# Optimization experiments

Measured on AMD Instinct MI355X. Metric: run time of the kernel, lower is better.

Reference implementation:

```python
import jax, jax.numpy as jnp
import numpy as np

N_HEADS = 16
MAX_SEQ_LEN = 2048


def _rotary_tables(d_k, max_seq_len):
    # Rotary.__init__: dim//4 frequencies followed by dim//4 zeros -> dim//2 entries
    freqs = (1.0 / 10000.0) ** jnp.linspace(0.0, 1.0, d_k // 4, dtype=jnp.float32)
    freqs = jnp.concatenate([freqs, jnp.zeros(d_k // 4, dtype=jnp.float32)])
    theta = jnp.arange(max_seq_len, dtype=jnp.float32)[:, None] * freqs[None, :]  # [S, d_k//2]
    return jnp.cos(theta), jnp.sin(theta)


def _apply_rotary_bug_faithful(u, cos, sin):
    # u: [B, H, T, Dk]. Original Rotary indexes cos/sin by u.size(-3) == n_heads,
    # so the rotation angle depends on the HEAD index and broadcasts over time.
    H = u.shape[1]
    c = cos[None, :H, None, :]  # [1, H, 1, Dk//2]
    s = sin[None, :H, None, :]
    u1, u2 = jnp.split(u.astype(jnp.float32), 2, axis=-1)
    y1 = u1 * c + u2 * s
    y2 = -u1 * s + u2 * c
    return jnp.concatenate([y1, y2], axis=-1).astype(u.dtype)


def setup_inputs() -> dict:
    key = jax.random.key(0)
    k1, k2, k3 = jax.random.split(key, 3)
    d_model = 2048
    B, T = 2, 2048
    x = jax.random.normal(k1, (B, T, d_model), dtype=jnp.float32)
    w_qkv = jax.random.normal(k2, (3 * d_model, d_model), dtype=jnp.float32) * (1.0 / np.sqrt(d_model))
    w_o = jax.random.normal(k3, (d_model, d_model), dtype=jnp.float32) * (1.0 / np.sqrt(d_model))
    return {"x": x, "w_qkv": w_qkv, "w_o": w_o}


def reference(x, w_qkv, w_o):
    B, T, D = x.shape
    H = N_HEADS
    dk = D // H
    cos, sin = _rotary_tables(dk, MAX_SEQ_LEN)

    # Fused QKV projection (Linear, no bias): [B,T,3D]
    qkv = jnp.einsum('btd,ed->bte', x, w_qkv)
    qkv = qkv.reshape(B, T, 3, H, dk).transpose(2, 0, 3, 1, 4)  # [3,B,H,T,dk]
    Q, K, V = qkv[0], qkv[1], qkv[2]

    Q = _apply_rotary_bug_faithful(Q, cos, sin)
    K = _apply_rotary_bug_faithful(K, cos, sin)

    # Causal scaled dot-product attention (eval mode -> dropout_p = 0)
    scale = 1.0 / np.sqrt(dk)
    scores = jnp.einsum('bhqd,bhkd->bhqk', Q, K) * scale
    causal = jnp.tril(jnp.ones((T, T), dtype=bool))
    scores = jnp.where(causal[None, None], scores, jnp.finfo(scores.dtype).min)
    attn = jax.nn.softmax(scores, axis=-1)
    out = jnp.einsum('bhqk,bhkd->bhqd', attn, V)  # [B,H,T,dk]
    out = out.transpose(0, 2, 1, 3).reshape(B, T, D)
    return jnp.einsum('btd,ed->bte', out, w_o)
```

## Files before the change

kernel.cpp:

```cpp
#include <hip/hip_runtime.h>

typedef unsigned short u16;
typedef short bf16x8 __attribute__((ext_vector_type(8)));
typedef float f32x4 __attribute__((ext_vector_type(4)));
typedef unsigned short u16x4 __attribute__((ext_vector_type(4)));

#define QK_SCALE 0.08838834764831845f

__device__ __forceinline__ u16 f2bf(float f) {
  unsigned u = __float_as_uint(f);
  u += 0x7fffu + ((u >> 16) & 1u);
  return (u16)(u >> 16);
}
__device__ __forceinline__ float bf2f(u16 h) { return __uint_as_float(((unsigned)h) << 16); }

__device__ __forceinline__ void gld_lds16(const u16* g, u16* l) {
  __builtin_amdgcn_global_load_lds(
      (const __attribute__((address_space(1))) void*)g,
      (__attribute__((address_space(3))) void*)l, 16, 0, 0);
}

__global__ void cvt_bf16_kernel(const float* __restrict__ in, u16* __restrict__ out, int n4) {
  int i = blockIdx.x * 256 + threadIdx.x;
  if (i >= n4) return;
  const float4 v = reinterpret_cast<const float4*>(in)[i];
  u16x4 o;
  o[0] = f2bf(v.x); o[1] = f2bf(v.y); o[2] = f2bf(v.z); o[3] = f2bf(v.w);
  reinterpret_cast<u16x4*>(out)[i] = o;
}

template<int MODE>
__global__ __launch_bounds__(512, 2) void gemm8p_kernel(
    const u16* __restrict__ A, const u16* __restrict__ Bw, int Kdim, int n_out,
    u16* __restrict__ q_out, u16* __restrict__ k_out, u16* __restrict__ v_out,
    float* __restrict__ f_out)
{
  __shared__ __align__(16) u16 As[2][256 * 64];
  __shared__ __align__(16) u16 Bs[2][256 * 64];
  const int t = threadIdx.x, lane = t & 63, w = t >> 6;
  const int wr = w >> 2, wc = w & 3;
  const int l15 = lane & 15, lhi = lane >> 4;
  const int m0 = blockIdx.x * 256, n0 = blockIdx.y * 256;
  const int NT = Kdim >> 6;

  const int srow = w * 8 + (lane >> 3);
  const int gchunk = (lane & 7) ^ (srow & 7);
  const size_t gcol = (size_t)gchunk * 8;

  auto stageA2 = [&](int buf, int kt2, int half) {
    const size_t kb = (size_t)kt2 * 64 + gcol;
#pragma unroll
    for (int i = 0; i < 2; ++i) {
      const int ro = half * 128 + i * 64;
      gld_lds16(A + (size_t)(m0 + srow + ro) * Kdim + kb, &As[buf][(w * 8 + ro) * 64]);
    }
  };
  auto stageB4 = [&](int buf, int kt2) {
    const size_t kb = (size_t)kt2 * 64 + gcol;
#pragma unroll
    for (int ro = 0; ro < 256; ro += 64)
      gld_lds16(Bw + (size_t)(n0 + srow + ro) * Kdim + kb, &Bs[buf][(w * 8 + ro) * 64]);
  };

  const int arow0 = (wr * 128 + l15) * 64;
  const int brow0 = (wc * 64 + l15) * 64;
  const int koff0 = ((0 + lhi) ^ (l15 & 7)) * 8;
  const int koff1 = ((4 + lhi) ^ (l15 & 7)) * 8;

  f32x4 acc[8][4];
#pragma unroll
  for (int m = 0; m < 8; ++m)
#pragma unroll
    for (int n = 0; n < 4; ++n)
#pragma unroll
      for (int i = 0; i < 4; ++i) acc[m][n][i] = 0.0f;

  stageA2(0, 0, 0); stageA2(0, 0, 1);
  stageB4(0, 0);
  if (NT > 1) { stageA2(1, 1, 0); stageA2(1, 1, 1); }
  asm volatile("s_waitcnt vmcnt(4)" ::: "memory");
  __builtin_amdgcn_s_barrier();

  for (int kt = 0; kt < NT; ++kt) {
    const int cur = kt & 1;
    const u16* __restrict__ Ac = &As[cur][0];
    const u16* __restrict__ Bc = &Bs[cur][0];
    bf16x8 aK1[4], a2K1[4], b0[4], b1[4];
    {
      bf16x8 aK0[4];
#pragma unroll
      for (int m = 0; m < 4; ++m) {
        aK0[m] = *reinterpret_cast<const bf16x8*>(Ac + arow0 + m * 1024 + koff0);
        aK1[m] = *reinterpret_cast<const bf16x8*>(Ac + arow0 + m * 1024 + koff1);
      }
#pragma unroll
      for (int n = 0; n < 4; ++n)
        b0[n] = *reinterpret_cast<const bf16x8*>(Bc + brow0 + n * 1024 + koff0);
      if (kt + 1 < NT) stageB4(cur ^ 1, kt + 1);
      __builtin_amdgcn_s_barrier();
      asm volatile("s_waitcnt lgkmcnt(0)" ::: "memory");
      __builtin_amdgcn_s_setprio(1);
#pragma unroll
      for (int m = 0; m < 4; ++m)
#pragma unroll
        for (int n = 0; n < 4; ++n)
          acc[m][n] = __builtin_amdgcn_mfma_f32_16x16x32_bf16(aK0[m], b0[n], acc[m][n], 0, 0, 0);
      __builtin_amdgcn_s_setprio(0);
      __builtin_amdgcn_s_barrier();
    }
    {
      bf16x8 a2K0[4];
#pragma unroll
      for (int m = 0; m < 4; ++m) {
        a2K0[m] = *reinterpret_cast<const bf16x8*>(Ac + arow0 + (m + 4) * 1024 + koff0);
        a2K1[m] = *reinterpret_cast<const bf16x8*>(Ac + arow0 + (m + 4) * 1024 + koff1);
      }
#pragma unroll
      for (int n = 0; n < 4; ++n)
        b1[n] = *reinterpret_cast<const bf16x8*>(Bc + brow0 + n * 1024 + koff1);
      __builtin_amdgcn_s_barrier();
      asm volatile("s_waitcnt lgkmcnt(0)" ::: "memory");
      __builtin_amdgcn_s_setprio(1);
#pragma unroll
      for (int m = 0; m < 4; ++m)
#pragma unroll
        for (int n = 0; n < 4; ++n)
          acc[m + 4][n] = __builtin_amdgcn_mfma_f32_16x16x32_bf16(a2K0[m], b0[n], acc[m + 4][n], 0, 0, 0);
      __builtin_amdgcn_s_setprio(0);
      __builtin_amdgcn_s_barrier();
    }
    if (kt + 2 < NT) stageA2(cur, kt + 2, 0);
    __builtin_amdgcn_s_barrier();
    __builtin_amdgcn_s_setprio(1);
#pragma unroll
    for (int m = 0; m < 4; ++m)
#pragma unroll
      for (int n = 0; n < 4; ++n)
        acc[m][n] = __builtin_amdgcn_mfma_f32_16x16x32_bf16(aK1[m], b1[n], acc[m][n], 0, 0, 0);
    __builtin_amdgcn_s_setprio(0);
    __builtin_amdgcn_s_barrier();
    if (kt + 2 < NT) stageA2(cur, kt + 2, 1);
    __builtin_amdgcn_s_barrier();
    __builtin_amdgcn_s_setprio(1);
#pragma unroll
    for (int m = 0; m < 4; ++m)
#pragma unroll
      for (int n = 0; n < 4; ++n)
        acc[m + 4][n] = __builtin_amdgcn_mfma_f32_16x16x32_bf16(a2K1[m], b1[n], acc[m + 4][n], 0, 0, 0);
    __builtin_amdgcn_s_setprio(0);
    if (kt < NT - 2) { asm volatile("s_waitcnt vmcnt(4)" ::: "memory"); }
    else             { asm volatile("s_waitcnt vmcnt(0)" ::: "memory"); }
    __builtin_amdgcn_s_barrier();
  }

  const int rb = wr * 128 + lhi * 4;
  const int cb = wc * 64 + l15;
  if (MODE == 0) {
#pragma unroll
    for (int n = 0; n < 4; ++n) {
      const int e = n0 + cb + n * 16;
      const int which = e >> 11;
      const int h = (e >> 7) & 15;
      const int d = e & 127;
      u16* dst = (which == 0) ? q_out : (which == 1) ? k_out : v_out;
#pragma unroll
      for (int m = 0; m < 8; ++m)
#pragma unroll
        for (int r = 0; r < 4; ++r) {
          const int bt = m0 + rb + m * 16 + r;
          const int bb = bt >> 11, tt = bt & 2047;
          dst[((size_t)(bb * 16 + h) * 2048 + tt) * 128 + d] = f2bf(acc[m][n][r]);
        }
    }
  } else {
#pragma unroll
    for (int m = 0; m < 8; ++m)
#pragma unroll
      for (int r = 0; r < 4; ++r) {
        const int row = m0 + rb + m * 16 + r;
#pragma unroll
        for (int n = 0; n < 4; ++n)
          f_out[(size_t)row * n_out + n0 + cb + n * 16] = acc[m][n][r];
      }
  }
}

__global__ __launch_bounds__(256) void gemm_bt_kernel(
    const u16* __restrict__ A, const u16* __restrict__ Bw, int Kdim, int n_out,
    float* __restrict__ f_out)
{
  __shared__ __align__(16) u16 Asl[128 * 32];
  __shared__ __align__(16) u16 Bsl[128 * 32];
  const int t = threadIdx.x;
  const int lane = t & 63;
  const int w = t >> 6;
  const int wr = w >> 1, wc = w & 1;
  const int m0 = blockIdx.x * 128, n0 = blockIdx.y * 128;

  f32x4 acc[4][4];
#pragma unroll
  for (int m = 0; m < 4; ++m)
#pragma unroll
    for (int n = 0; n < 4; ++n)
#pragma unroll
      for (int i = 0; i < 4; ++i) acc[m][n][i] = 0.0f;

  const int ob0 = w * 1024 + lane * 16;
  const int row0 = ob0 >> 6;
  const int cole0 = (ob0 & 63) >> 1;
  const u16* gA0 = A + (size_t)(m0 + row0) * Kdim + cole0;
  const u16* gA1 = gA0 + (size_t)64 * Kdim;
  const u16* gB0 = Bw + (size_t)(n0 + row0) * Kdim + cole0;
  const u16* gB1 = gB0 + (size_t)64 * Kdim;
  u16* lA = Asl + w * 512;
  u16* lB = Bsl + w * 512;

  const int l15 = lane & 15;
  const int kb = (lane >> 4) * 8;

  for (int k0 = 0; k0 < Kdim; k0 += 32) {
    __syncthreads();
    gld_lds16(gA0, lA);
    gld_lds16(gA1, lA + 2048);
    gld_lds16(gB0, lB);
    gld_lds16(gB1, lB + 2048);
    gA0 += 32; gA1 += 32; gB0 += 32; gB1 += 32;
    __syncthreads();
    bf16x8 a[4], b[4];
#pragma unroll
    for (int m = 0; m < 4; ++m)
      a[m] = *reinterpret_cast<const bf16x8*>(Asl + (wr * 64 + m * 16 + l15) * 32 + kb);
#pragma unroll
    for (int n = 0; n < 4; ++n)
      b[n] = *reinterpret_cast<const bf16x8*>(Bsl + (wc * 64 + n * 16 + l15) * 32 + kb);
#pragma unroll
    for (int m = 0; m < 4; ++m)
#pragma unroll
      for (int n = 0; n < 4; ++n)
        acc[m][n] = __builtin_amdgcn_mfma_f32_16x16x32_bf16(a[m], b[n], acc[m][n], 0, 0, 0);
  }

  const int rb = wr * 64 + ((lane >> 4) << 2);
  const int cbs = wc * 64 + l15;
#pragma unroll
  for (int m = 0; m < 4; ++m)
#pragma unroll
    for (int r = 0; r < 4; ++r) {
      const int row = m0 + rb + m * 16 + r;
#pragma unroll
      for (int n = 0; n < 4; ++n)
        f_out[(size_t)row * n_out + n0 + cbs + n * 16] = acc[m][n][r];
    }
}

__global__ void rotary_kernel(u16* __restrict__ Qb, u16* __restrict__ Kb) {
  const int idx = blockIdx.x * 256 + threadIdx.x;
  const int j4 = idx & 15;
  const int row = idx >> 4;
  const int h = (row >> 11) & 15;
  const size_t base = (size_t)row * 128 + j4 * 4;
  float c[4], s[4];
#pragma unroll
  for (int i = 0; i < 4; ++i) {
    const int j = j4 * 4 + i;
    const float fr = (j < 32) ? __expf(-0.2971077539f * (float)j) : 0.0f;
    const float th = (float)h * fr;
    c[i] = cosf(th); s[i] = sinf(th);
  }
  {
    u16x4 u1 = *reinterpret_cast<u16x4*>(Qb + base);
    u16x4 u2 = *reinterpret_cast<u16x4*>(Qb + base + 64);
    u16x4 y1, y2;
#pragma unroll
    for (int i = 0; i < 4; ++i) {
      const float a = bf2f(u1[i]), b = bf2f(u2[i]);
      y1[i] = f2bf((a * c[i] + b * s[i]) * QK_SCALE);
      y2[i] = f2bf((b * c[i] - a * s[i]) * QK_SCALE);
    }
    *reinterpret_cast<u16x4*>(Qb + base) = y1;
    *reinterpret_cast<u16x4*>(Qb + base + 64) = y2;
  }
  {
    u16x4 u1 = *reinterpret_cast<u16x4*>(Kb + base);
    u16x4 u2 = *reinterpret_cast<u16x4*>(Kb + base + 64);
    u16x4 y1, y2;
#pragma unroll
    for (int i = 0; i < 4; ++i) {
      const float a = bf2f(u1[i]), b = bf2f(u2[i]);
      y1[i] = f2bf(a * c[i] + b * s[i]);
      y2[i] = f2bf(b * c[i] - a * s[i]);
    }
    *reinterpret_cast<u16x4*>(Kb + base) = y1;
    *reinterpret_cast<u16x4*>(Kb + base + 64) = y2;
  }
}

__global__ void transpose_v_kernel(const u16* __restrict__ V, u16* __restrict__ Vt) {
  __shared__ u16 tile[64][65];
  const int d0 = blockIdx.x * 64;
  const int t0 = blockIdx.y * 64;
  const int bh = blockIdx.z;
  const u16* src = V + (size_t)bh * (2048 * 128);
  u16* dst = Vt + (size_t)bh * (128 * 2048);
  const int tid = threadIdx.x;
  const int c4 = (tid & 15) * 4;
  const int r0 = tid >> 4;
#pragma unroll
  for (int p = 0; p < 4; ++p) {
    const int row = r0 + p * 16;
    const u16x4 v = *reinterpret_cast<const u16x4*>(src + (size_t)(t0 + row) * 128 + d0 + c4);
    tile[row][c4] = v[0]; tile[row][c4 + 1] = v[1];
    tile[row][c4 + 2] = v[2]; tile[row][c4 + 3] = v[3];
  }
  __syncthreads();
#pragma unroll
  for (int p = 0; p < 4; ++p) {
    const int dr = r0 + p * 16;
    u16x4 ov;
    ov[0] = tile[c4][dr]; ov[1] = tile[c4 + 1][dr];
    ov[2] = tile[c4 + 2][dr]; ov[3] = tile[c4 + 3][dr];
    *reinterpret_cast<u16x4*>(dst + (size_t)(d0 + dr) * 2048 + t0 + c4) = ov;
  }
}

__global__ __launch_bounds__(256) void attn_kernel(
    const u16* __restrict__ Q, const u16* __restrict__ K,
    const u16* __restrict__ Vt, u16* __restrict__ O)
{
  __shared__ __align__(16) u16 k_lds[2][64 * 128];
  __shared__ __align__(16) u16 v_lds[2][128 * 64];
  __shared__ __align__(16) u16 p_lds[4][1024];
  const int t = threadIdx.x, lane = t & 63, w = t >> 6;
  const int bh = blockIdx.y;
  const int bx = blockIdx.x;
  const int l15 = lane & 15, lhi = lane >> 4;
  const size_t qkb = (size_t)bh * (2048 * 128);
  const u16* Kg = K + qkb;
  const u16* Vg = Vt + (size_t)bh * (size_t)(128 * 2048);
  char* pw = (char*)(&p_lds[w][0]);
  const int bb = bh >> 4, h = bh & 15;
  const int kxor = (l15 & 7) << 4;

  auto stage = [&](int buf, int k0) {
#pragma unroll
    for (int ii = 0; ii < 4; ++ii) {
      const int i = w * 4 + ii;
      const int krow = i * 4 + lhi;
      gld_lds16(Kg + (size_t)(k0 + krow) * 128 + (size_t)((l15 ^ (krow & 7)) * 8),
                &k_lds[buf][i * 512]);
    }
#pragma unroll
    for (int ii = 0; ii < 4; ++ii) {
      const int i = w * 4 + ii;
      const int vrow = i * 8 + (lane >> 3);
      gld_lds16(Vg + (size_t)vrow * 2048 + k0 + (size_t)(((lane & 7) ^ (vrow & 7)) * 8),
                &v_lds[buf][i * 512]);
    }
  };

  for (int half = 0; half < 2; ++half) {
    const int qt = half ? (31 - bx) : bx;
    const int q0 = qt * 64 + w * 16;
    bf16x8 aq[4];
    {
      const u16* qp = Q + qkb + (size_t)(q0 + l15) * 128 + lhi * 8;
#pragma unroll
      for (int ks = 0; ks < 4; ++ks) aq[ks] = *reinterpret_cast<const bf16x8*>(qp + ks * 32);
    }
    f32x4 o[8];
#pragma unroll
    for (int dt = 0; dt < 8; ++dt)
#pragma unroll
      for (int i = 0; i < 4; ++i) o[dt][i] = 0.0f;
    float mrow[4] = {-1e30f, -1e30f, -1e30f, -1e30f};
    float lrow[4] = {0.f, 0.f, 0.f, 0.f};
    const int rbase = q0 + (lhi << 2);
    const int ktmax = qt;

    __syncthreads();
    stage(0, 0);
    int cur = 0;
    for (int kt = 0; kt <= ktmax; ++kt) {
      __syncthreads();
      if (kt < ktmax) stage(cur ^ 1, (kt + 1) * 64);

      const char* kbb = (const char*)(&k_lds[cur][0]);
      f32x4 s4[4];
#pragma unroll
      for (int nt = 0; nt < 4; ++nt)
#pragma unroll
        for (int i = 0; i < 4; ++i) s4[nt][i] = 0.0f;
#pragma unroll
      for (int nt = 0; nt < 4; ++nt) {
        const int krow = nt * 16 + l15;
#pragma unroll
        for (int ks = 0; ks < 4; ++ks) {
          const bf16x8 bk = *reinterpret_cast<const bf16x8*>(
              kbb + krow * 256 + ((ks * 64 + lhi * 16) ^ kxor));
          s4[nt] = __builtin_amdgcn_mfma_f32_16x16x32_bf16(aq[ks], bk, s4[nt], 0, 0, 0);
        }
      }
      if (kt == ktmax) {
#pragma unroll
        for (int nt = 0; nt < 4; ++nt) {
          const int col = kt * 64 + nt * 16 + l15;
#pragma unroll
          for (int r = 0; r < 4; ++r)
            if (col > rbase + r) s4[nt][r] = -1e30f;
        }
      }
      float alpha[4];
#pragma unroll
      for (int r = 0; r < 4; ++r) {
        float mx = fmaxf(fmaxf(s4[0][r], s4[1][r]), fmaxf(s4[2][r], s4[3][r]));
        mx = fmaxf(mx, __shfl_xor(mx, 1));
        mx = fmaxf(mx, __shfl_xor(mx, 2));
        mx = fmaxf(mx, __shfl_xor(mx, 4));
        mx = fmaxf(mx, __shfl_xor(mx, 8));
        const float mn = fmaxf(mrow[r], mx);
        alpha[r] = __expf(mrow[r] - mn);
        mrow[r] = mn;
      }
      float ps[4] = {0.f, 0.f, 0.f, 0.f};
#pragma unroll
      for (int nt = 0; nt < 4; ++nt)
#pragma unroll
        for (int r = 0; r < 4; ++r) {
          const float p = __expf(s4[nt][r] - mrow[r]);
          ps[r] += p;
          const int prow = (lhi << 2) + r;
          const int cbyte = (nt * 16 + l15) * 2;
          *(u16*)(pw + prow * 128 + (cbyte ^ ((prow & 7) << 4))) = f2bf(p);
        }
#pragma unroll
      for (int r = 0; r < 4; ++r) {
        float rs = ps[r];
        rs += __shfl_xor(rs, 1);
        rs += __shfl_xor(rs, 2);
        rs += __shfl_xor(rs, 4);
        rs += __shfl_xor(rs, 8);
        lrow[r] = lrow[r] * alpha[r] + rs;
#pragma unroll
        for (int dt = 0; dt < 8; ++dt) o[dt][r] *= alpha[r];
      }
      const char* vbb = (const char*)(&v_lds[cur][0]);
#pragma unroll
      for (int ks2 = 0; ks2 < 2; ++ks2) {
        const bf16x8 ap = *reinterpret_cast<const bf16x8*>(
            pw + l15 * 128 + ((ks2 * 64 + (lhi << 4)) ^ kxor));
#pragma unroll
        for (int dt = 0; dt < 8; ++dt) {
          const int vrow = dt * 16 + l15;
          const bf16x8 bv = *reinterpret_cast<const bf16x8*>(
              vbb + vrow * 128 + ((ks2 * 64 + lhi * 16) ^ kxor));
          o[dt] = __builtin_amdgcn_mfma_f32_16x16x32_bf16(ap, bv, o[dt], 0, 0, 0);
        }
      }
      cur ^= 1;
    }
#pragma unroll
    for (int r = 0; r < 4; ++r) {
      const float inv = 1.0f / lrow[r];
      const int row = rbase + r;
      u16* op = O + (size_t)(bb * 2048 + row) * 2048 + h * 128 + l15;
#pragma unroll
      for (int dt = 0; dt < 8; ++dt) op[dt * 16] = f2bf(o[dt][r] * inv);
    }
  }
}

extern "C" void kernel_launch(void* const* d_in, const int* in_sizes, int n_in,
                              void* d_out, int out_size, void* d_ws, size_t ws_size,
                              hipStream_t stream) {
  const float* x = (const float*)d_in[0];
  const float* wqkv = (const float*)d_in[1];
  const float* wo = (const float*)d_in[2];
  float* out = (float*)d_out;
  u16* ws = (u16*)d_ws;

  u16* xb = ws;
  u16* wqkvb = xb + 8388608;
  u16* wob = wqkvb + 12582912;
  u16* Qb = wob + 4194304;
  u16* Kb = Qb + 8388608;
  u16* Vb = Kb + 8388608;
  u16* Vtb = wqkvb;
  u16* attn = xb;

  cvt_bf16_kernel<<<8192, 256, 0, stream>>>(x, xb, 2097152);
  cvt_bf16_kernel<<<12288, 256, 0, stream>>>(wqkv, wqkvb, 3145728);
  cvt_bf16_kernel<<<4096, 256, 0, stream>>>(wo, wob, 1048576);

  gemm8p_kernel<0><<<dim3(16, 24), 512, 0, stream>>>(xb, wqkvb, 2048, 0, Qb, Kb, Vb, nullptr);

  rotary_kernel<<<4096, 256, 0, stream>>>(Qb, Kb);
  transpose_v_kernel<<<dim3(2, 32, 32), 256, 0, stream>>>(Vb, Vtb);

  attn_kernel<<<dim3(16, 32), 256, 0, stream>>>(Qb, Kb, Vtb, attn);

  gemm_bt_kernel<<<dim3(32, 16), 256, 0, stream>>>(attn, wob, 2048, 2048, out);
}
```

Measured before the change: 323.3 us.

## Fold rotary into QKV weights, write V transposed from GEMM, swizzle block order

New measurement: 346.7 us. 1.07x slower.

```diff
diff --git a/kernel.cpp b/kernel.cpp
--- a/kernel.cpp
+++ b/kernel.cpp
@@ -27,6 +27,33 @@
   u16x4 o;
   o[0] = f2bf(v.x); o[1] = f2bf(v.y); o[2] = f2bf(v.z); o[3] = f2bf(v.w);
   reinterpret_cast<u16x4*>(out)[i] = o;
+}
+
+__global__ void rotw_kernel(const float* __restrict__ w, u16* __restrict__ wb) {
+  const int i = blockIdx.x * 256 + threadIdx.x;
+  const int k4 = i & 511;
+  const int j = (i >> 9) & 63;
+  const int h = (i >> 15) & 15;
+  const int which = i >> 19;
+  const size_t e1 = (size_t)which * 2048 + h * 128 + j;
+  const size_t e2 = e1 + 64;
+  const float fr = (j < 32) ? __expf(-0.2971077539f * (float)j) : 0.0f;
+  float s, c;
+  __sincosf((float)h * fr, &s, &c);
+  const float scale = (which == 0) ? QK_SCALE : 1.0f;
+  const float4 a = reinterpret_cast<const float4*>(w + e1 * 2048)[k4];
+  const float4 b = reinterpret_cast<const float4*>(w + e2 * 2048)[k4];
+  u16x4 o1, o2;
+  o1[0] = f2bf((a.x * c + b.x * s) * scale);
+  o1[1] = f2bf((a.y * c + b.y * s) * scale);
+  o1[2] = f2bf((a.z * c + b.z * s) * scale);
+  o1[3] = f2bf((a.w * c + b.w * s) * scale);
+  o2[0] = f2bf((b.x * c - a.x * s) * scale);
+  o2[1] = f2bf((b.y * c - a.y * s) * scale);
+  o2[2] = f2bf((b.z * c - a.z * s) * scale);
+  o2[3] = f2bf((b.w * c - a.w * s) * scale);
+  reinterpret_cast<u16x4*>(wb + e1 * 2048)[k4] = o1;
+  reinterpret_cast<u16x4*>(wb + e2 * 2048)[k4] = o2;
 }
 
 template<int MODE>
@@ -40,7 +67,9 @@
   const int t = threadIdx.x, lane = t & 63, w = t >> 6;
   const int wr = w >> 2, wc = w & 3;
   const int l15 = lane & 15, lhi = lane >> 4;
-  const int m0 = blockIdx.x * 256, n0 = blockIdx.y * 256;
+  const int flat = blockIdx.y * 16 + blockIdx.x;
+  const int swz = (flat & 7) * 48 + (flat >> 3);
+  const int m0 = (swz & 15) << 8, n0 = (swz >> 4) << 8;
   const int NT = Kdim >> 6;
 
   const int srow = w * 8 + (lane >> 3);
@@ -162,14 +191,19 @@
       const int which = e >> 11;
       const int h = (e >> 7) & 15;
       const int d = e & 127;
-      u16* dst = (which == 0) ? q_out : (which == 1) ? k_out : v_out;
 #pragma unroll
       for (int m = 0; m < 8; ++m)
 #pragma unroll
         for (int r = 0; r < 4; ++r) {
           const int bt = m0 + rb + m * 16 + r;
           const int bb = bt >> 11, tt = bt & 2047;
-          dst[((size_t)(bb * 16 + h) * 2048 + tt) * 128 + d] = f2bf(acc[m][n][r]);
+          const float val = acc[m][n][r];
+          if (which == 2) {
+            v_out[((size_t)(bb * 16 + h) * 128 + d) * 2048 + tt] = f2bf(val);
+          } else {
+            u16* dst = (which == 0) ? q_out : k_out;
+            dst[((size_t)(bb * 16 + h) * 2048 + tt) * 128 + d] = f2bf(val);
+          }
         }
     }
   } else {
@@ -195,7 +229,9 @@
   const int lane = t & 63;
   const int w = t >> 6;
   const int wr = w >> 1, wc = w & 1;
-  const int m0 = blockIdx.x * 128, n0 = blockIdx.y * 128;
+  const int flat = blockIdx.y * 32 + blockIdx.x;
+  const int swz = (flat & 7) * 64 + (flat >> 3);
+  const int m0 = (swz & 31) << 7, n0 = (swz >> 5) << 7;
 
   f32x4 acc[4][4];
 #pragma unroll
@@ -253,76 +289,6 @@
     }
 }
 
-__global__ void rotary_kernel(u16* __restrict__ Qb, u16* __restrict__ Kb) {
-  const int idx = blockIdx.x * 256 + threadIdx.x;
-  const int j4 = idx & 15;
-  const int row = idx >> 4;
-  const int h = (row >> 11) & 15;
-  const size_t base = (size_t)row * 128 + j4 * 4;
-  float c[4], s[4];
-#pragma unroll
-  for (int i = 0; i < 4; ++i) {
-    const int j = j4 * 4 + i;
-    const float fr = (j < 32) ? __expf(-0.2971077539f * (float)j) : 0.0f;
-    const float th = (float)h * fr;
-    c[i] = cosf(th); s[i] = sinf(th);
-  }
-  {
-    u16x4 u1 = *reinterpret_cast<u16x4*>(Qb + base);
-    u16x4 u2 = *reinterpret_cast<u16x4*>(Qb + base + 64);
-    u16x4 y1, y2;
-#pragma unroll
-    for (int i = 0; i < 4; ++i) {
-      const float a = bf2f(u1[i]), b = bf2f(u2[i]);
-      y1[i] = f2bf((a * c[i] + b * s[i]) * QK_SCALE);
-      y2[i] = f2bf((b * c[i] - a * s[i]) * QK_SCALE);
-    }
-    *reinterpret_cast<u16x4*>(Qb + base) = y1;
-    *reinterpret_cast<u16x4*>(Qb + base + 64) = y2;
-  }
-  {
-    u16x4 u1 = *reinterpret_cast<u16x4*>(Kb + base);
-    u16x4 u2 = *reinterpret_cast<u16x4*>(Kb + base + 64);
-    u16x4 y1, y2;
-#pragma unroll
-    for (int i = 0; i < 4; ++i) {
-      const float a = bf2f(u1[i]), b = bf2f(u2[i]);
-      y1[i] = f2bf(a * c[i] + b * s[i]);
-      y2[i] = f2bf(b * c[i] - a * s[i]);
-    }
-    *reinterpret_cast<u16x4*>(Kb + base) = y1;
-    *reinterpret_cast<u16x4*>(Kb + base + 64) = y2;
-  }
-}
-
-__global__ void transpose_v_kernel(const u16* __restrict__ V, u16* __restrict__ Vt) {
-  __shared__ u16 tile[64][65];
-  const int d0 = blockIdx.x * 64;
-  const int t0 = blockIdx.y * 64;
-  const int bh = blockIdx.z;
-  const u16* src = V + (size_t)bh * (2048 * 128);
-  u16* dst = Vt + (size_t)bh * (128 * 2048);
-  const int tid = threadIdx.x;
-  const int c4 = (tid & 15) * 4;
-  const int r0 = tid >> 4;
-#pragma unroll
-  for (int p = 0; p < 4; ++p) {
-    const int row = r0 + p * 16;
-    const u16x4 v = *reinterpret_cast<const u16x4*>(src + (size_t)(t0 + row) * 128 + d0 + c4);
-    tile[row][c4] = v[0]; tile[row][c4 + 1] = v[1];
-    tile[row][c4 + 2] = v[2]; tile[row][c4 + 3] = v[3];
-  }
-  __syncthreads();
-#pragma unroll
-  for (int p = 0; p < 4; ++p) {
-    const int dr = r0 + p * 16;
-    u16x4 ov;
-    ov[0] = tile[c4][dr]; ov[1] = tile[c4 + 1][dr];
-    ov[2] = tile[c4 + 2][dr]; ov[3] = tile[c4 + 3][dr];
-    *reinterpret_cast<u16x4*>(dst + (size_t)(d0 + dr) * 2048 + t0 + c4) = ov;
-  }
-}
-
 __global__ __launch_bounds__(256) void attn_kernel(
     const u16* __restrict__ Q, const u16* __restrict__ K,
     const u16* __restrict__ Vt, u16* __restrict__ O)
@@ -331,8 +297,10 @@
   __shared__ __align__(16) u16 v_lds[2][128 * 64];
   __shared__ __align__(16) u16 p_lds[4][1024];
   const int t = threadIdx.x, lane = t & 63, w = t >> 6;
-  const int bh = blockIdx.y;
-  const int bx = blockIdx.x;
+  const int flat = blockIdx.y * 16 + blockIdx.x;
+  const int swz = (flat & 7) * 64 + (flat >> 3);
+  const int bx = swz & 15;
+  const int bh = swz >> 4;
   const int l15 = lane & 15, lhi = lane >> 4;
   const size_t qkb = (size_t)bh * (2048 * 128);
   const u16* Kg = K + qkb;
@@ -483,18 +451,16 @@
   u16* wob = wqkvb + 12582912;
   u16* Qb = wob + 4194304;
   u16* Kb = Qb + 8388608;
-  u16* Vb = Kb + 8388608;
-  u16* Vtb = wqkvb;
+  u16* Vtb = Kb + 8388608;
   u16* attn = xb;
 
   cvt_bf16_kernel<<<8192, 256, 0, stream>>>(x, xb, 2097152);
-  cvt_bf16_kernel<<<12288, 256, 0, stream>>>(wqkv, wqkvb, 3145728);
+  rotw_kernel<<<4096, 256, 0, stream>>>(wqkv, wqkvb);
+  cvt_bf16_kernel<<<4096, 256, 0, stream>>>(wqkv + (size_t)4096 * 2048,
+                                            wqkvb + (size_t)4096 * 2048, 1048576);
   cvt_bf16_kernel<<<4096, 256, 0, stream>>>(wo, wob, 1048576);
 
-  gemm8p_kernel<0><<<dim3(16, 24), 512, 0, stream>>>(xb, wqkvb, 2048, 0, Qb, Kb, Vb, nullptr);
-
-  rotary_kernel<<<4096, 256, 0, stream>>>(Qb, Kb);
-  transpose_v_kernel<<<dim3(2, 32, 32), 256, 0, stream>>>(Vb, Vtb);
+  gemm8p_kernel<0><<<dim3(16, 24), 512, 0, stream>>>(xb, wqkvb, 2048, 0, Qb, Kb, Vtb, nullptr);
 
   attn_kernel<<<dim3(16, 32), 256, 0, stream>>>(Qb, Kb, Vtb, attn);
 
```
